# Performance work log

Measured on AMD Instinct MI355X. Metric: run time of the kernel, lower is better.

## Reference

```python
import jax, jax.numpy as jnp
import numpy as np

WS = (7, 7, 7)          # window size (S, H, W)
DIM = 192
HEADS = 6
BW = 256                # B_ = batch * num_windows
N = WS[0] * WS[1] * WS[2]  # 343 tokens per window


def _relative_position_index(ws):
    # Faithful reproduction of the torch buffer construction.
    coords = np.stack(np.meshgrid(np.arange(ws[0]), np.arange(ws[1]), np.arange(ws[2]), indexing='ij'))
    flat = coords.reshape(3, -1)                      # [3, N]
    rel = flat[:, :, None] - flat[:, None, :]         # [3, N, N]
    rel = rel.transpose(1, 2, 0).astype(np.int32)     # [N, N, 3]
    rel[..., 0] += ws[0] - 1
    rel[..., 1] += ws[1] - 1
    rel[..., 2] += ws[2] - 1
    rel[..., 0] *= (2 * ws[1] - 1) * (2 * ws[2] - 1)
    rel[..., 1] *= 2 * ws[2] - 1
    return rel.sum(-1)                                # [N, N] in [0, (2ws-1)^3)


def setup_inputs() -> dict:
    key = jax.random.key(0)
    ks = jax.random.split(key, 6)
    table_size = (2 * WS[0] - 1) * (2 * WS[1] - 1) * (2 * WS[2] - 1)  # 2197
    return {
        'x': jax.random.normal(ks[0], (BW, N, DIM), dtype=jnp.float32),
        'w_qkv': jax.random.normal(ks[1], (3 * DIM, DIM), dtype=jnp.float32) * 0.02,
        'b_qkv': jnp.zeros((3 * DIM,), dtype=jnp.float32),
        'w_proj': jax.random.normal(ks[2], (DIM, DIM), dtype=jnp.float32) * 0.02,
        'b_proj': jnp.zeros((DIM,), dtype=jnp.float32),
        'bias_table': jax.random.normal(ks[3], (table_size, HEADS), dtype=jnp.float32) * 0.02,
        'rel_index': jnp.asarray(_relative_position_index(WS)),  # [N, N] int32
        'is_global': 0,
    }


def reference(x, w_qkv, b_qkv, w_proj, b_proj, bias_table, rel_index, is_global):
    # x: [B_, N, C]; dropout rates are 0 (eval), is_global=0 -> local window path.
    B_, n, C = x.shape
    H = HEADS
    hd = C // H
    scale = jnp.asarray(hd, x.dtype) ** -0.5

    qkv = x @ w_qkv.T + b_qkv                         # [B_, N, 3C]
    qkv = qkv.reshape(B_, n, 3, H, hd)
    q = qkv[:, :, 0].transpose(0, 2, 1, 3) * scale    # [B_, H, N, hd]
    k = qkv[:, :, 1].transpose(0, 2, 1, 3)
    v = qkv[:, :, 2].transpose(0, 2, 1, 3)

    attn = jnp.einsum('bhqd,bhkd->bhqk', q, k)        # [B_, H, N, N]
    bias = bias_table[rel_index]                      # gather: [N, N, H]
    attn = attn + bias.transpose(2, 0, 1)[None]       # add per-head relative bias
    attn = jax.nn.softmax(attn, axis=-1)

    out = jnp.einsum('bhqk,bhkd->bhqd', attn, v)      # [B_, H, N, hd]
    out = out.transpose(0, 2, 1, 3).reshape(B_, n, C)
    return out @ w_proj.T + b_proj                    # [B_, N, C]
```

## Files before the change

kernel.cpp:

```cpp
#include <hip/hip_runtime.h>
#include <hip/hip_bf16.h>

#define BWIN 256
#define NTOK 343
#define CDIM 192
#define NH   6
#define HD   32
#define QKVF 576
#define NROWS (BWIN * NTOK)
#define SCALE 0.17677669529663687f
#define LOG2E 1.4426950408889634f

typedef unsigned short u16;
typedef unsigned int   u32;
typedef short bf16x8 __attribute__((ext_vector_type(8)));
typedef float f32x4 __attribute__((ext_vector_type(4)));
typedef unsigned short u16x8 __attribute__((ext_vector_type(8)));

#define OFF_QKVB 0UL
#define OFF_OPB  101154816UL
#define OFF_WQB  101154816UL
#define OFF_BQS  101376000UL
#define OFF_BMB  134873088UL
#define OFF_WPB  136359936UL
#define WS_NEED  136433664UL

__device__ __forceinline__ u16 f2bf(float f) {
    u32 u = __float_as_uint(f);
    u += 0x7FFFu + ((u >> 16) & 1u);
    return (u16)(u >> 16);
}
__device__ __forceinline__ float bf2f(u16 h) {
    return __uint_as_float(((u32)h) << 16);
}
__device__ __forceinline__ u32 pk2bf(float a, float b) {
    union { __hip_bfloat162 h; u32 u; } v;
    v.h = __float22bfloat162_rn(make_float2(a, b));
    return v.u;
}

__global__ void ws_too_small_sentinel(float* out) { out[0] = 1.0e6f; }

__global__ __launch_bounds__(256) void cvt_small(
    const float* __restrict__ wq, const float* __restrict__ wp,
    const float* __restrict__ bq, const float* __restrict__ btab,
    const int* __restrict__ ridx,
    u16* __restrict__ wqb, u16* __restrict__ wpb,
    float* __restrict__ bqs, u16* __restrict__ bmb)
{
    const int i = blockIdx.x * 256 + threadIdx.x;
    if (i < 110592) {
        const int fb = i / 3072;
        const int r1 = i - fb * 3072;
        const int kk = r1 >> 9;
        const int t  = r1 & 511;
        const int lane = t >> 3, e = t & 7;
        const int row = fb * 16 + (lane & 15);
        const int k   = kk * 32 + (lane >> 4) * 8 + e;
        wqb[i] = f2bf(wq[row * 192 + k] * (row < CDIM ? SCALE * LOG2E : 1.0f));
    } else if (i < 147456) {
        const int u = i - 110592;
        const int fb = u / 3072;
        const int r1 = u - fb * 3072;
        const int kk = r1 >> 9;
        const int t  = r1 & 511;
        const int lane = t >> 3, e = t & 7;
        const int row = fb * 16 + (lane & 15);
        const int k   = kk * 32 + (lane >> 4) * 8 + e;
        wpb[u] = f2bf(wp[row * 192 + k]);
    } else if (i < 148032) {
        const int f = i - 147456;
        bqs[f] = bq[f] * (f < CDIM ? SCALE * LOG2E : 1.0f);
    } else if (i < 891456) {
        const int u = i - 148032;
        const int hh = u / 123904;
        const int rem = u - hh * 123904;
        const int qt = rem / 5632;
        const int rem2 = rem - qt * 5632;
        const int jc = rem2 >> 9;
        const int t = rem2 & 511;
        const int lane = t >> 3, e = t & 7;
        const int cl = lane & 15, g = lane >> 4;
        const int q = min(qt * 16 + cl, NTOK - 1);
        const int j = jc * 32 + ((e < 4) ? (g * 4 + e) : (16 + g * 4 + (e - 4)));
        const float v = (j < NTOK) ? btab[ridx[q * NTOK + j] * NH + hh] * LOG2E
                                   : -10000.0f;
        bmb[u] = f2bf(v);
    }
}

__global__ __launch_bounds__(256, 4) void gemm_qkv(
    const float* __restrict__ x, const u16* __restrict__ wqb,
    const float* __restrict__ bqs, u16* __restrict__ qkvb)
{
    __shared__ __align__(16) u16 Xs[64 * 200];
    __shared__ __align__(16) u16 Ct[64 * 104];
    const int m0 = blockIdx.x * 64;
    const int tid = threadIdx.x;
    const int wave = tid >> 6, lane = tid & 63, g = lane >> 4, cl = lane & 15;
    const int wm = (wave >> 1) * 32, wf = (wave & 1) * 48;

    #pragma unroll
    for (int p = 0; p < 12; ++p) {
        const int u = tid + 256 * p;
        const int row = u / 48, c = u - row * 48;
        const float4 v = *(const float4*)(x + (size_t)(m0 + row) * CDIM + c * 4);
        *(uint2*)(Xs + row * 200 + c * 4) = make_uint2(pk2bf(v.x, v.y), pk2bf(v.z, v.w));
    }
    __syncthreads();

    for (int fc = 0; fc < 6; ++fc) {
        const int f0 = fc * 96;
        f32x4 acc[2][3];
        #pragma unroll
        for (int t = 0; t < 2; ++t)
            #pragma unroll
            for (int s = 0; s < 3; ++s) acc[t][s] = (f32x4){0.f, 0.f, 0.f, 0.f};

        const u16* wbase = wqb + (size_t)(fc * 6 + (wave & 1) * 3) * 3072 + lane * 8;
        #pragma unroll
        for (int kk = 0; kk < 6; ++kk) {
            const int kcol = kk * 32;
            bf16x8 a[2], bb[3];
            #pragma unroll
            for (int s = 0; s < 3; ++s)
                bb[s] = *(const bf16x8*)(wbase + s * 3072 + kk * 512);
            #pragma unroll
            for (int t = 0; t < 2; ++t)
                a[t] = *(const bf16x8*)(Xs + (wm + t * 16 + cl) * 200 + kcol + g * 8);
            #pragma unroll
            for (int t = 0; t < 2; ++t)
                #pragma unroll
                for (int s = 0; s < 3; ++s)
                    acc[t][s] = __builtin_amdgcn_mfma_f32_16x16x32_bf16(a[t], bb[s], acc[t][s], 0, 0, 0);
        }

        __syncthreads();
        #pragma unroll
        for (int s = 0; s < 3; ++s) {
            const float bv = bqs[f0 + wf + s * 16 + cl];
            #pragma unroll
            for (int t = 0; t < 2; ++t) {
                const int row = wm + t * 16 + g * 4;
                const int col = wf + s * 16 + cl;
                const u32 p01 = pk2bf(acc[t][s][0] + bv, acc[t][s][1] + bv);
                const u32 p23 = pk2bf(acc[t][s][2] + bv, acc[t][s][3] + bv);
                Ct[(row + 0) * 104 + col] = (u16)p01;
                Ct[(row + 1) * 104 + col] = (u16)(p01 >> 16);
                Ct[(row + 2) * 104 + col] = (u16)p23;
                Ct[(row + 3) * 104 + col] = (u16)(p23 >> 16);
            }
        }
        __syncthreads();
        #pragma unroll
        for (int p = 0; p < 3; ++p) {
            const int u = tid + 256 * p;
            const int row = u / 12, c = u - row * 12;
            *(float4*)(qkvb + (size_t)(m0 + row) * QKVF + f0 + c * 8) =
                *(const float4*)(Ct + row * 104 + c * 8);
        }
    }
}

__global__ __launch_bounds__(256, 4) void attn_mfma(
    const u16* __restrict__ qkvb, const u16* __restrict__ bmb,
    u16* __restrict__ opb)
{
    __shared__ u16 Vt[HD][360];
    __shared__ u16 Os[4][16][32];
    const int b = blockIdx.x, h = blockIdx.y;
    const int tid = threadIdx.x;
    const int wave = tid >> 6, lane = tid & 63, g = lane >> 4, cl = lane & 15;
    const size_t rowbase = (size_t)b * NTOK;

    for (int u = tid; u < 1408; u += 256) {
        const int row = u >> 2, seg = u & 3;
        union { float4 f; u16 hx[8]; } vv;
        vv.f = make_float4(0.f, 0.f, 0.f, 0.f);
        if (row < NTOK)
            vv.f = *(const float4*)(qkvb + (rowbase + row) * QKVF + 2 * CDIM + h * HD + seg * 8);
        const int jl = row & 31;
        const int slot = (jl < 16) ? ((jl >> 2) << 3) + (jl & 3)
                                   : (((jl - 16) >> 2) << 3) + 4 + (jl & 3);
        const int pcol = (row & ~31) + slot;
        #pragma unroll
        for (int e = 0; e < 8; ++e) Vt[seg * 8 + e][pcol] = vv.hx[e];
    }
    __syncthreads();

    bf16x8 ones;
    #pragma unroll
    for (int e = 0; e < 8; ++e) ones[e] = (short)0x3F80;

    for (int base = wave * 2; base < 22; base += 8) {
        const int q0a = base * 16, q0b = q0a + 16;
        const bf16x8 qa0 = *(const bf16x8*)(qkvb + (rowbase + min(q0a + cl, NTOK - 1)) * QKVF + h * HD + g * 8);
        const bf16x8 qa1 = *(const bf16x8*)(qkvb + (rowbase + min(q0b + cl, NTOK - 1)) * QKVF + h * HD + g * 8);
        const u16* bpA = bmb + ((size_t)(h * 22 + base) * 11) * 512 + lane * 8;
        const u16* bpB = bpA + 5632;

        bf16x8 kb0 = *(const bf16x8*)(qkvb + (rowbase + cl) * QKVF + CDIM + h * HD + g * 8);
        bf16x8 kb1 = *(const bf16x8*)(qkvb + (rowbase + 16 + cl) * QKVF + CDIM + h * HD + g * 8);
        u16x8 bA = *(const u16x8*)(bpA);
        u16x8 bB = *(const u16x8*)(bpB);

        f32x4 oA0 = {0,0,0,0}, oA1 = {0,0,0,0}, lA = {0,0,0,0};
        f32x4 oB0 = {0,0,0,0}, oB1 = {0,0,0,0}, lB = {0,0,0,0};

        for (int jc = 0; jc < 11; ++jc) {
            const int j0 = jc * 32;
            const bf16x8 ck0 = kb0, ck1 = kb1;
            const u16x8 cA = bA, cB = bB;
            if (jc < 10) {
                const int jn = j0 + 32;
                kb0 = *(const bf16x8*)(qkvb + (rowbase + min(jn + cl, NTOK - 1)) * QKVF + CDIM + h * HD + g * 8);
                kb1 = *(const bf16x8*)(qkvb + (rowbase + min(jn + 16 + cl, NTOK - 1)) * QKVF + CDIM + h * HD + g * 8);
                bA = *(const u16x8*)(bpA + (jc + 1) * 512);
                bB = *(const u16x8*)(bpB + (jc + 1) * 512);
            }
            const bf16x8 vb0 = *(const bf16x8*)&Vt[cl][j0 + g * 8];
            const bf16x8 vb1 = *(const bf16x8*)&Vt[16 + cl][j0 + g * 8];

            {
                f32x4 c0 = { bf2f(cA[0]), bf2f(cA[1]), bf2f(cA[2]), bf2f(cA[3]) };
                f32x4 c1 = { bf2f(cA[4]), bf2f(cA[5]), bf2f(cA[6]), bf2f(cA[7]) };
                const f32x4 s0 = __builtin_amdgcn_mfma_f32_16x16x32_bf16(ck0, qa0, c0, 0, 0, 0);
                const f32x4 s1 = __builtin_amdgcn_mfma_f32_16x16x32_bf16(ck1, qa0, c1, 0, 0, 0);
                union { bf16x8 v; u32 w[4]; } pa;
                pa.w[0] = pk2bf(__builtin_amdgcn_exp2f(s0[0]), __builtin_amdgcn_exp2f(s0[1]));
                pa.w[1] = pk2bf(__builtin_amdgcn_exp2f(s0[2]), __builtin_amdgcn_exp2f(s0[3]));
                pa.w[2] = pk2bf(__builtin_amdgcn_exp2f(s1[0]), __builtin_amdgcn_exp2f(s1[1]));
                pa.w[3] = pk2bf(__builtin_amdgcn_exp2f(s1[2]), __builtin_amdgcn_exp2f(s1[3]));
                oA0 = __builtin_amdgcn_mfma_f32_16x16x32_bf16(pa.v, vb0, oA0, 0, 0, 0);
                oA1 = __builtin_amdgcn_mfma_f32_16x16x32_bf16(pa.v, vb1, oA1, 0, 0, 0);
                lA  = __builtin_amdgcn_mfma_f32_16x16x32_bf16(pa.v, ones, lA, 0, 0, 0);
            }
            {
                f32x4 c0 = { bf2f(cB[0]), bf2f(cB[1]), bf2f(cB[2]), bf2f(cB[3]) };
                f32x4 c1 = { bf2f(cB[4]), bf2f(cB[5]), bf2f(cB[6]), bf2f(cB[7]) };
                const f32x4 s0 = __builtin_amdgcn_mfma_f32_16x16x32_bf16(ck0, qa1, c0, 0, 0, 0);
                const f32x4 s1 = __builtin_amdgcn_mfma_f32_16x16x32_bf16(ck1, qa1, c1, 0, 0, 0);
                union { bf16x8 v; u32 w[4]; } pa;
                pa.w[0] = pk2bf(__builtin_amdgcn_exp2f(s0[0]), __builtin_amdgcn_exp2f(s0[1]));
                pa.w[1] = pk2bf(__builtin_amdgcn_exp2f(s0[2]), __builtin_amdgcn_exp2f(s0[3]));
                pa.w[2] = pk2bf(__builtin_amdgcn_exp2f(s1[0]), __builtin_amdgcn_exp2f(s1[1]));
                pa.w[3] = pk2bf(__builtin_amdgcn_exp2f(s1[2]), __builtin_amdgcn_exp2f(s1[3]));
                oB0 = __builtin_amdgcn_mfma_f32_16x16x32_bf16(pa.v, vb0, oB0, 0, 0, 0);
                oB1 = __builtin_amdgcn_mfma_f32_16x16x32_bf16(pa.v, vb1, oB1, 0, 0, 0);
                lB  = __builtin_amdgcn_mfma_f32_16x16x32_bf16(pa.v, ones, lB, 0, 0, 0);
            }
        }
        #pragma unroll
        for (int half = 0; half < 2; ++half) {
            const f32x4 o0 = half ? oB0 : oA0;
            const f32x4 o1 = half ? oB1 : oA1;
            const f32x4 lc = half ? lB : lA;
            const int q0 = half ? q0b : q0a;
            #pragma unroll
            for (int r = 0; r < 4; ++r) {
                const float inv = 1.0f / lc[r];
                Os[wave][g * 4 + r][cl]      = f2bf(o0[r] * inv);
                Os[wave][g * 4 + r][16 + cl] = f2bf(o1[r] * inv);
            }
            const int row = lane >> 2, cg = (lane & 3) * 8;
            const int q = q0 + row;
            if (q < NTOK)
                *(float4*)(opb + (rowbase + q) * CDIM + h * HD + cg) =
                    *(const float4*)&Os[wave][row][cg];
        }
    }
}

__global__ __launch_bounds__(256, 3) void gemm_proj(
    const u16* __restrict__ opb, const u16* __restrict__ wpb,
    const float* __restrict__ bp, float* __restrict__ out)
{
    __shared__ __align__(16) u16 smem[128 * 200];
    u16*   Xs = smem;
    float* Cf = (float*)smem;
    const int f0 = blockIdx.x * 96, m0 = blockIdx.y * 128;
    const int tid = threadIdx.x;
    const int wave = tid >> 6, lane = tid & 63, g = lane >> 4, cl = lane & 15;
    const int wm = (wave >> 1) * 64, wf = (wave & 1) * 48;

    #pragma unroll
    for (int p = 0; p < 12; ++p) {
        const int u = tid + 256 * p;
        const int row = u / 24, c = u - row * 24;
        *(float4*)(Xs + row * 200 + c * 8) =
            *(const float4*)(opb + (size_t)(m0 + row) * CDIM + c * 8);
    }
    __syncthreads();

    f32x4 acc[4][3];
    #pragma unroll
    for (int t = 0; t < 4; ++t)
        #pragma unroll
        for (int s = 0; s < 3; ++s) acc[t][s] = (f32x4){0.f, 0.f, 0.f, 0.f};

    const u16* wbase = wpb + (size_t)(blockIdx.x * 6 + (wave & 1) * 3) * 3072 + lane * 8;
    #pragma unroll
    for (int kk = 0; kk < 6; ++kk) {
        const int kcol = kk * 32;
        bf16x8 a[4], bb[3];
        #pragma unroll
        for (int s = 0; s < 3; ++s)
            bb[s] = *(const bf16x8*)(wbase + s * 3072 + kk * 512);
        #pragma unroll
        for (int t = 0; t < 4; ++t)
            a[t] = *(const bf16x8*)(Xs + (wm + t * 16 + cl) * 200 + kcol + g * 8);
        #pragma unroll
        for (int t = 0; t < 4; ++t)
            #pragma unroll
            for (int s = 0; s < 3; ++s)
                acc[t][s] = __builtin_amdgcn_mfma_f32_16x16x32_bf16(a[t], bb[s], acc[t][s], 0, 0, 0);
    }

    #pragma unroll
    for (int half = 0; half < 2; ++half) {
        __syncthreads();
        if ((wave >> 1) == half) {
            #pragma unroll
            for (int s = 0; s < 3; ++s) {
                const float bv = bp[f0 + wf + s * 16 + cl];
                #pragma unroll
                for (int t = 0; t < 4; ++t)
                    #pragma unroll
                    for (int r = 0; r < 4; ++r)
                        Cf[(t * 16 + g * 4 + r) * 104 + wf + s * 16 + cl] = acc[t][s][r] + bv;
            }
        }
        __syncthreads();
        #pragma unroll
        for (int p = 0; p < 6; ++p) {
            const int u = tid + 256 * p;
            const int row = u / 24, c = u - row * 24;
            *(float4*)(out + (size_t)(m0 + half * 64 + row) * CDIM + f0 + c * 4) =
                *(const float4*)(Cf + row * 104 + c * 4);
        }
    }
}

extern "C" void kernel_launch(void* const* d_in, const int* in_sizes, int n_in,
                              void* d_out, int out_size, void* d_ws, size_t ws_size,
                              hipStream_t stream) {
    const float* x     = (const float*)d_in[0];
    const float* wqkv  = (const float*)d_in[1];
    const float* bqkv  = (const float*)d_in[2];
    const float* wproj = (const float*)d_in[3];
    const float* bproj = (const float*)d_in[4];
    const float* btab  = (const float*)d_in[5];
    const int*   ridx  = (const int*)d_in[6];
    float* out = (float*)d_out;

    if (ws_size < WS_NEED) {
        hipLaunchKernelGGL(ws_too_small_sentinel, dim3(1), dim3(1), 0, stream, out);
        return;
    }
    char* ws = (char*)d_ws;
    u16*   qkvb = (u16*)(ws + OFF_QKVB);
    u16*   wqb  = (u16*)(ws + OFF_WQB);
    u16*   wpb  = (u16*)(ws + OFF_WPB);
    float* bqs  = (float*)(ws + OFF_BQS);
    u16*   bmb  = (u16*)(ws + OFF_BMB);
    u16*   opb  = (u16*)(ws + OFF_OPB);

    hipLaunchKernelGGL(cvt_small, dim3(3483), dim3(256), 0, stream,
                       wqkv, wproj, bqkv, btab, ridx, wqb, wpb, bqs, bmb);
    hipLaunchKernelGGL(gemm_qkv, dim3(NROWS / 64), dim3(256), 0, stream,
                       x, wqb, bqs, qkvb);
    hipLaunchKernelGGL(attn_mfma, dim3(BWIN, NH), dim3(256), 0, stream,
                       qkvb, bmb, opb);
    hipLaunchKernelGGL(gemm_proj, dim3(2, NROWS / 128), dim3(256), 0, stream,
                       opb, wpb, bproj, out);
}
```

Measured before the change: 255.9 us.

## Deepen K/bias prefetch in attention loop and retile projection GEMM per 64 rows

The attention inner loop is manually unrolled by two so the K fragments and bias tiles are prefetched two chunks ahead instead of one, which should hide more global-load latency. The projection GEMM now has each block handle 64 rows across both 96-column output halves. Each block reads its activation tile into LDS once instead of once per column half, and separate LDS buffers replace the aliased staging buffer. The cost is higher register pressure in attention and more sequential work per projection block.

```diff
diff --git a/kernel.cpp b/kernel.cpp
--- a/kernel.cpp
+++ b/kernel.cpp
@@ -162,6 +162,43 @@
     }
 }
 
+#define LDK(ROW) (*(const bf16x8*)(qkvb + (rowbase + min(ROW, NTOK - 1)) * QKVF + CDIM + h * HD + g * 8))
+#define LDBA(JC) (*(const u16x8*)(bpA + (JC) * 512))
+#define LDBB(JC) (*(const u16x8*)(bpB + (JC) * 512))
+
+#define JCBODY(J0, CK0, CK1, CA, CB) do {                                            \
+    const bf16x8 vb0 = *(const bf16x8*)&Vt[cl][(J0) + g * 8];                        \
+    const bf16x8 vb1 = *(const bf16x8*)&Vt[16 + cl][(J0) + g * 8];                   \
+    {                                                                                \
+        f32x4 c0 = { bf2f((CA)[0]), bf2f((CA)[1]), bf2f((CA)[2]), bf2f((CA)[3]) };   \
+        f32x4 c1 = { bf2f((CA)[4]), bf2f((CA)[5]), bf2f((CA)[6]), bf2f((CA)[7]) };   \
+        const f32x4 s0 = __builtin_amdgcn_mfma_f32_16x16x32_bf16(CK0, qa0, c0, 0, 0, 0); \
+        const f32x4 s1 = __builtin_amdgcn_mfma_f32_16x16x32_bf16(CK1, qa0, c1, 0, 0, 0); \
+        union { bf16x8 v; u32 w[4]; } pa;                                            \
+        pa.w[0] = pk2bf(__builtin_amdgcn_exp2f(s0[0]), __builtin_amdgcn_exp2f(s0[1])); \
+        pa.w[1] = pk2bf(__builtin_amdgcn_exp2f(s0[2]), __builtin_amdgcn_exp2f(s0[3])); \
+        pa.w[2] = pk2bf(__builtin_amdgcn_exp2f(s1[0]), __builtin_amdgcn_exp2f(s1[1])); \
+        pa.w[3] = pk2bf(__builtin_amdgcn_exp2f(s1[2]), __builtin_amdgcn_exp2f(s1[3])); \
+        oA0 = __builtin_amdgcn_mfma_f32_16x16x32_bf16(pa.v, vb0, oA0, 0, 0, 0);      \
+        oA1 = __builtin_amdgcn_mfma_f32_16x16x32_bf16(pa.v, vb1, oA1, 0, 0, 0);      \
+        lA  = __builtin_amdgcn_mfma_f32_16x16x32_bf16(pa.v, ones, lA, 0, 0, 0);      \
+    }                                                                                \
+    {                                                                                \
+        f32x4 c0 = { bf2f((CB)[0]), bf2f((CB)[1]), bf2f((CB)[2]), bf2f((CB)[3]) };   \
+        f32x4 c1 = { bf2f((CB)[4]), bf2f((CB)[5]), bf2f((CB)[6]), bf2f((CB)[7]) };   \
+        const f32x4 s0 = __builtin_amdgcn_mfma_f32_16x16x32_bf16(CK0, qa1, c0, 0, 0, 0); \
+        const f32x4 s1 = __builtin_amdgcn_mfma_f32_16x16x32_bf16(CK1, qa1, c1, 0, 0, 0); \
+        union { bf16x8 v; u32 w[4]; } pa;                                            \
+        pa.w[0] = pk2bf(__builtin_amdgcn_exp2f(s0[0]), __builtin_amdgcn_exp2f(s0[1])); \
+        pa.w[1] = pk2bf(__builtin_amdgcn_exp2f(s0[2]), __builtin_amdgcn_exp2f(s0[3])); \
+        pa.w[2] = pk2bf(__builtin_amdgcn_exp2f(s1[0]), __builtin_amdgcn_exp2f(s1[1])); \
+        pa.w[3] = pk2bf(__builtin_amdgcn_exp2f(s1[2]), __builtin_amdgcn_exp2f(s1[3])); \
+        oB0 = __builtin_amdgcn_mfma_f32_16x16x32_bf16(pa.v, vb0, oB0, 0, 0, 0);      \
+        oB1 = __builtin_amdgcn_mfma_f32_16x16x32_bf16(pa.v, vb1, oB1, 0, 0, 0);      \
+        lB  = __builtin_amdgcn_mfma_f32_16x16x32_bf16(pa.v, ones, lB, 0, 0, 0);      \
+    }                                                                                \
+} while (0)
+
 __global__ __launch_bounds__(256, 4) void attn_mfma(
     const u16* __restrict__ qkvb, const u16* __restrict__ bmb,
     u16* __restrict__ opb)
@@ -199,57 +236,35 @@
         const u16* bpA = bmb + ((size_t)(h * 22 + base) * 11) * 512 + lane * 8;
         const u16* bpB = bpA + 5632;
 
-        bf16x8 kb0 = *(const bf16x8*)(qkvb + (rowbase + cl) * QKVF + CDIM + h * HD + g * 8);
-        bf16x8 kb1 = *(const bf16x8*)(qkvb + (rowbase + 16 + cl) * QKVF + CDIM + h * HD + g * 8);
-        u16x8 bA = *(const u16x8*)(bpA);
-        u16x8 bB = *(const u16x8*)(bpB);
+        bf16x8 k0a = LDK(cl),      k0b = LDK(16 + cl);
+        u16x8  b0A = LDBA(0),      b0B = LDBB(0);
+        bf16x8 k1a = LDK(32 + cl), k1b = LDK(48 + cl);
+        u16x8  b1A = LDBA(1),      b1B = LDBB(1);
 
         f32x4 oA0 = {0,0,0,0}, oA1 = {0,0,0,0}, lA = {0,0,0,0};
         f32x4 oB0 = {0,0,0,0}, oB1 = {0,0,0,0}, lB = {0,0,0,0};
 
-        for (int jc = 0; jc < 11; ++jc) {
-            const int j0 = jc * 32;
-            const bf16x8 ck0 = kb0, ck1 = kb1;
-            const u16x8 cA = bA, cB = bB;
-            if (jc < 10) {
-                const int jn = j0 + 32;
-                kb0 = *(const bf16x8*)(qkvb + (rowbase + min(jn + cl, NTOK - 1)) * QKVF + CDIM + h * HD + g * 8);
-                kb1 = *(const bf16x8*)(qkvb + (rowbase + min(jn + 16 + cl, NTOK - 1)) * QKVF + CDIM + h * HD + g * 8);
-                bA = *(const u16x8*)(bpA + (jc + 1) * 512);
-                bB = *(const u16x8*)(bpB + (jc + 1) * 512);
+        #pragma unroll
+        for (int p = 0; p < 5; ++p) {
+            {
+                const int jc2 = 2 * p + 2;
+                const bf16x8 nka = LDK(jc2 * 32 + cl), nkb = LDK(jc2 * 32 + 16 + cl);
+                const u16x8  nA  = LDBA(jc2),          nB  = LDBB(jc2);
+                JCBODY(2 * p * 32, k0a, k0b, b0A, b0B);
+                k0a = nka; k0b = nkb; b0A = nA; b0B = nB;
             }
-            const bf16x8 vb0 = *(const bf16x8*)&Vt[cl][j0 + g * 8];
-            const bf16x8 vb1 = *(const bf16x8*)&Vt[16 + cl][j0 + g * 8];
-
-            {
-                f32x4 c0 = { bf2f(cA[0]), bf2f(cA[1]), bf2f(cA[2]), bf2f(cA[3]) };
-                f32x4 c1 = { bf2f(cA[4]), bf2f(cA[5]), bf2f(cA[6]), bf2f(cA[7]) };
-                const f32x4 s0 = __builtin_amdgcn_mfma_f32_16x16x32_bf16(ck0, qa0, c0, 0, 0, 0);
-                const f32x4 s1 = __builtin_amdgcn_mfma_f32_16x16x32_bf16(ck1, qa0, c1, 0, 0, 0);
-                union { bf16x8 v; u32 w[4]; } pa;
-                pa.w[0] = pk2bf(__builtin_amdgcn_exp2f(s0[0]), __builtin_amdgcn_exp2f(s0[1]));
-                pa.w[1] = pk2bf(__builtin_amdgcn_exp2f(s0[2]), __builtin_amdgcn_exp2f(s0[3]));
-                pa.w[2] = pk2bf(__builtin_amdgcn_exp2f(s1[0]), __builtin_amdgcn_exp2f(s1[1]));
-                pa.w[3] = pk2bf(__builtin_amdgcn_exp2f(s1[2]), __builtin_amdgcn_exp2f(s1[3]));
-                oA0 = __builtin_amdgcn_mfma_f32_16x16x32_bf16(pa.v, vb0, oA0, 0, 0, 0);
-                oA1 = __builtin_amdgcn_mfma_f32_16x16x32_bf16(pa.v, vb1, oA1, 0, 0, 0);
-                lA  = __builtin_amdgcn_mfma_f32_16x16x32_bf16(pa.v, ones, lA, 0, 0, 0);
+            if (2 * p + 3 <= 10) {
+                const int jc3 = 2 * p + 3;
+                const bf16x8 nka = LDK(jc3 * 32 + cl), nkb = LDK(jc3 * 32 + 16 + cl);
+                const u16x8  nA  = LDBA(jc3),          nB  = LDBB(jc3);
+                JCBODY((2 * p + 1) * 32, k1a, k1b, b1A, b1B);
+                k1a = nka; k1b = nkb; b1A = nA; b1B = nB;
+            } else {
+                JCBODY((2 * p + 1) * 32, k1a, k1b, b1A, b1B);
             }
-            {
-                f32x4 c0 = { bf2f(cB[0]), bf2f(cB[1]), bf2f(cB[2]), bf2f(cB[3]) };
-                f32x4 c1 = { bf2f(cB[4]), bf2f(cB[5]), bf2f(cB[6]), bf2f(cB[7]) };
-                const f32x4 s0 = __builtin_amdgcn_mfma_f32_16x16x32_bf16(ck0, qa1, c0, 0, 0, 0);
-                const f32x4 s1 = __builtin_amdgcn_mfma_f32_16x16x32_bf16(ck1, qa1, c1, 0, 0, 0);
-                union { bf16x8 v; u32 w[4]; } pa;
-                pa.w[0] = pk2bf(__builtin_amdgcn_exp2f(s0[0]), __builtin_amdgcn_exp2f(s0[1]));
-                pa.w[1] = pk2bf(__builtin_amdgcn_exp2f(s0[2]), __builtin_amdgcn_exp2f(s0[3]));
-                pa.w[2] = pk2bf(__builtin_amdgcn_exp2f(s1[0]), __builtin_amdgcn_exp2f(s1[1]));
-                pa.w[3] = pk2bf(__builtin_amdgcn_exp2f(s1[2]), __builtin_amdgcn_exp2f(s1[3]));
-                oB0 = __builtin_amdgcn_mfma_f32_16x16x32_bf16(pa.v, vb0, oB0, 0, 0, 0);
-                oB1 = __builtin_amdgcn_mfma_f32_16x16x32_bf16(pa.v, vb1, oB1, 0, 0, 0);
-                lB  = __builtin_amdgcn_mfma_f32_16x16x32_bf16(pa.v, ones, lB, 0, 0, 0);
-            }
-        }
+        }
+        JCBODY(320, k0a, k0b, b0A, b0B);
+
         #pragma unroll
         for (int half = 0; half < 2; ++half) {
             const f32x4 o0 = half ? oB0 : oA0;
@@ -275,16 +290,15 @@
     const u16* __restrict__ opb, const u16* __restrict__ wpb,
     const float* __restrict__ bp, float* __restrict__ out)
 {
-    __shared__ __align__(16) u16 smem[128 * 200];
-    u16*   Xs = smem;
-    float* Cf = (float*)smem;
-    const int f0 = blockIdx.x * 96, m0 = blockIdx.y * 128;
+    __shared__ __align__(16) u16 Xs[64 * 200];
+    __shared__ __align__(16) float Cf[64 * 104];
+    const int m0 = blockIdx.x * 64;
     const int tid = threadIdx.x;
     const int wave = tid >> 6, lane = tid & 63, g = lane >> 4, cl = lane & 15;
-    const int wm = (wave >> 1) * 64, wf = (wave & 1) * 48;
+    const int wm = (wave >> 1) * 32, wf = (wave & 1) * 48;
 
     #pragma unroll
-    for (int p = 0; p < 12; ++p) {
+    for (int p = 0; p < 6; ++p) {
         const int u = tid + 256 * p;
         const int row = u / 24, c = u - row * 24;
         *(float4*)(Xs + row * 200 + c * 8) =
@@ -292,50 +306,48 @@
     }
     __syncthreads();
 
-    f32x4 acc[4][3];
-    #pragma unroll
-    for (int t = 0; t < 4; ++t)
-        #pragma unroll
-        for (int s = 0; s < 3; ++s) acc[t][s] = (f32x4){0.f, 0.f, 0.f, 0.f};
-
-    const u16* wbase = wpb + (size_t)(blockIdx.x * 6 + (wave & 1) * 3) * 3072 + lane * 8;
-    #pragma unroll
-    for (int kk = 0; kk < 6; ++kk) {
-        const int kcol = kk * 32;
-        bf16x8 a[4], bb[3];
-        #pragma unroll
-        for (int s = 0; s < 3; ++s)
-            bb[s] = *(const bf16x8*)(wbase + s * 3072 + kk * 512);
-        #pragma unroll
-        for (int t = 0; t < 4; ++t)
-            a[t] = *(const bf16x8*)(Xs + (wm + t * 16 + cl) * 200 + kcol + g * 8);
-        #pragma unroll
-        for (int t = 0; t < 4; ++t)
+    for (int fc = 0; fc < 2; ++fc) {
+        const int f0 = fc * 96;
+        f32x4 acc[2][3];
+        #pragma unroll
+        for (int t = 0; t < 2; ++t)
+            #pragma unroll
+            for (int s = 0; s < 3; ++s) acc[t][s] = (f32x4){0.f, 0.f, 0.f, 0.f};
+
+        const u16* wbase = wpb + (size_t)(fc * 6 + (wave & 1) * 3) * 3072 + lane * 8;
+        #pragma unroll
+        for (int kk = 0; kk < 6; ++kk) {
+            const int kcol = kk * 32;
+            bf16x8 a[2], bb[3];
             #pragma unroll
             for (int s = 0; s < 3; ++s)
-                acc[t][s] = __builtin_amdgcn_mfma_f32_16x16x32_bf16(a[t], bb[s], acc[t][s], 0, 0, 0);
-    }
-
-    #pragma unroll
-    for (int half = 0; half < 2; ++half) {
+                bb[s] = *(const bf16x8*)(wbase + s * 3072 + kk * 512);
+            #pragma unroll
+            for (int t = 0; t < 2; ++t)
+                a[t] = *(const bf16x8*)(Xs + (wm + t * 16 + cl) * 200 + kcol + g * 8);
+            #pragma unroll
+            for (int t = 0; t < 2; ++t)
+                #pragma unroll
+                for (int s = 0; s < 3; ++s)
+                    acc[t][s] = __builtin_amdgcn_mfma_f32_16x16x32_bf16(a[t], bb[s], acc[t][s], 0, 0, 0);
+        }
+
         __syncthreads();
-        if ((wave >> 1) == half) {
-            #pragma unroll
-            for (int s = 0; s < 3; ++s) {
-                const float bv = bp[f0 + wf + s * 16 + cl];
+        #pragma unroll
+        for (int s = 0; s < 3; ++s) {
+            const float bv = bp[f0 + wf + s * 16 + cl];
+            #pragma unroll
+            for (int t = 0; t < 2; ++t)
                 #pragma unroll
-                for (int t = 0; t < 4; ++t)
-                    #pragma unroll
-                    for (int r = 0; r < 4; ++r)
-                        Cf[(t * 16 + g * 4 + r) * 104 + wf + s * 16 + cl] = acc[t][s][r] + bv;
-            }
+                for (int r = 0; r < 4; ++r)
+                    Cf[(wm + t * 16 + g * 4 + r) * 104 + wf + s * 16 + cl] = acc[t][s][r] + bv;
         }
         __syncthreads();
         #pragma unroll
         for (int p = 0; p < 6; ++p) {
             const int u = tid + 256 * p;
             const int row = u / 24, c = u - row * 24;
-            *(float4*)(out + (size_t)(m0 + half * 64 + row) * CDIM + f0 + c * 4) =
+            *(float4*)(out + (size_t)(m0 + row) * CDIM + f0 + c * 4) =
                 *(const float4*)(Cf + row * 104 + c * 4);
         }
     }
@@ -371,6 +383,6 @@
                        x, wqb, bqs, qkvb);
     hipLaunchKernelGGL(attn_mfma, dim3(BWIN, NH), dim3(256), 0, stream,
                        qkvb, bmb, opb);
-    hipLaunchKernelGGL(gemm_proj, dim3(2, NROWS / 128), dim3(256), 0, stream,
+    hipLaunchKernelGGL(gemm_proj, dim3(NROWS / 64), dim3(256), 0, stream,
                        opb, wpb, bproj, out);
 }
```

New measurement: 397.3 us. 55.2% more time.
